# Kernel optimization log

Measured on AMD Instinct MI355X. Metric: run time of the kernel, lower is better.

## Reference

```python
import jax, jax.numpy as jnp
import numpy as np

N, C, B = 800000, 64, 8
BN_EPS = 1e-5


def setup_inputs() -> dict:
    key = jax.random.key(0)
    ks = jax.random.split(key, 8)
    x = jax.random.normal(ks[0], (N, C), dtype=jnp.float32)
    # cumulative end-offsets of B equal segments: [100000, 200000, ..., 800000]
    o = (jnp.arange(1, B + 1, dtype=jnp.int64) * (N // B))
    s2 = 1.0 / np.sqrt(C)
    s1 = 1.0 / np.sqrt(2 * C)
    w2 = jax.random.uniform(ks[1], (C, C), jnp.float32, -s2, s2)      # linear2 Linear(C,C)
    b2 = jax.random.uniform(ks[2], (C,), jnp.float32, -s2, s2)
    w1 = jax.random.uniform(ks[3], (C, 2 * C), jnp.float32, -s1, s1)  # linear1 Linear(2C,C)
    b1 = jax.random.uniform(ks[4], (C,), jnp.float32, -s1, s1)
    gamma = jnp.ones((C,), jnp.float32)   # BatchNorm1d weight
    beta = jnp.zeros((C,), jnp.float32)   # BatchNorm1d bias
    return {"x": x, "o": o, "w2": w2, "b2": b2, "w1": w1, "b1": b1,
            "gamma": gamma, "beta": beta}


def reference(x, o, w2, b2, w1, b1, gamma, beta):
    n = x.shape[0]
    nb = o.shape[0]
    # segment id of each point: point i belongs to segment j iff o[j-1] <= i < o[j]
    seg = jnp.searchsorted(o, jnp.arange(n), side="right")          # [N]
    counts = jnp.diff(o, prepend=0).astype(x.dtype)                  # [B]
    # per-segment mean pool
    means = jax.ops.segment_sum(x, seg, num_segments=nb) / counts[:, None]  # [B, C]
    # linear2: Linear + ReLU on pooled vectors
    h = jax.nn.relu(means @ w2.T + b2)                               # [B, C]
    # broadcast pooled features back to points and concat
    cat = jnp.concatenate([x, h[seg]], axis=1)                       # [N, 2C]
    # linear1: Linear + BatchNorm1d (training-mode batch stats) + ReLU
    y = cat @ w1.T + b1                                              # [N, C]
    mu = y.mean(axis=0)
    var = y.var(axis=0)
    y = (y - mu) * jax.lax.rsqrt(var + BN_EPS) * gamma + beta
    return jax.nn.relu(y)
```

## Files before the change

### kernel.cpp

```cpp
#include <hip/hip_runtime.h>

#define NROWS 800000
#define SEGROWS 100000
#define K1_BLOCKS 800
#define K1_ROWS 1000

typedef __attribute__((ext_vector_type(8))) short bf16x8;
typedef __attribute__((ext_vector_type(4))) float f32x4;
typedef __attribute__((ext_vector_type(4))) short short4v;

__device__ inline unsigned short f2bf(float f) {
    unsigned u = __builtin_bit_cast(unsigned, f);
    return (unsigned short)((u + 0x7FFFu + ((u >> 16) & 1u)) >> 16);
}

__global__ void kzero(float* __restrict__ p) {
    int t = blockIdx.x * 256 + threadIdx.x;
    if (t < 33280) p[t] = 0.f;
}

__global__ __launch_bounds__(256, 2)
void k1_stats(const float* __restrict__ x, float* __restrict__ m2p, float* __restrict__ ssumg)
{
    __shared__ __align__(16) float smem[5120];
    short* xt = (short*)smem;
    const float4* X4 = (const float4*)x;
    int t = threadIdx.x, w = t >> 6, lane = t & 63;
    int c4 = t & 15, g = t >> 4;
    size_t r0 = (size_t)blockIdx.x * K1_ROWS;
    int seg = (int)(r0 / SEGROWS);

    f32x4 acc[4][4];
#pragma unroll
    for (int p = 0; p < 4; ++p)
#pragma unroll
        for (int q = 0; q < 4; ++q) acc[p][q] = (f32x4){0.f, 0.f, 0.f, 0.f};
    float s0 = 0, s1 = 0, s2 = 0, s3 = 0;

    for (int tile = 0; tile < K1_ROWS; tile += 128) {
        int nr = min(128, K1_ROWS - tile);
        __syncthreads();
        if (nr == 128) {
            float4 v[8];
#pragma unroll
            for (int i = 0; i < 8; ++i)
                v[i] = X4[(r0 + tile + 8 * g + i) * 16 + c4];
#pragma unroll
            for (int i = 0; i < 8; ++i) {
                s0 += v[i].x; s1 += v[i].y; s2 += v[i].z; s3 += v[i].w;
            }
#pragma unroll
            for (int j = 0; j < 4; ++j) {
                bf16x8 pk;
#pragma unroll
                for (int i = 0; i < 8; ++i)
                    pk[i] = (short)f2bf(((const float*)&v[i])[j]);
                *(bf16x8*)&xt[(4 * c4 + j) * 136 + 8 * g] = pk;
            }
        } else {
#pragma unroll
            for (int h = 0; h < 2; ++h) {
                int rg = 8 * g + 4 * h;
                float4 v[4];
#pragma unroll
                for (int i = 0; i < 4; ++i) {
                    int r = rg + i;
                    if (r < nr) {
                        v[i] = X4[(r0 + tile + r) * 16 + c4];
                        s0 += v[i].x; s1 += v[i].y; s2 += v[i].z; s3 += v[i].w;
                    } else v[i] = make_float4(0.f, 0.f, 0.f, 0.f);
                }
#pragma unroll
                for (int j = 0; j < 4; ++j) {
                    short4v pk;
                    pk[0] = (short)f2bf(((const float*)&v[0])[j]);
                    pk[1] = (short)f2bf(((const float*)&v[1])[j]);
                    pk[2] = (short)f2bf(((const float*)&v[2])[j]);
                    pk[3] = (short)f2bf(((const float*)&v[3])[j]);
                    *(short4v*)&xt[(4 * c4 + j) * 136 + rg] = pk;
                }
            }
        }
        __syncthreads();
        bf16x8 f[4];
#pragma unroll
        for (int c0 = 0; c0 < 4; ++c0)
            f[c0] = *(const bf16x8*)&xt[(16 * c0 + (lane & 15)) * 136 + 32 * w + 8 * (lane >> 4)];
#pragma unroll
        for (int p = 0; p < 4; ++p)
#pragma unroll
            for (int q = 0; q < 4; ++q)
                acc[p][q] = __builtin_amdgcn_mfma_f32_16x16x32_bf16(f[p], f[q], acc[p][q], 0, 0, 0);
    }

    __syncthreads();
    ((float4*)(smem + 4096))[t] = make_float4(s0, s1, s2, s3);
    int qd = lane >> 4, cl = lane & 15;
    if (w == 0) {
#pragma unroll
        for (int p = 0; p < 4; ++p)
#pragma unroll
            for (int q = 0; q < 4; ++q)
#pragma unroll
                for (int i = 0; i < 4; ++i)
                    smem[(16 * p + 4 * qd + i) * 64 + 16 * q + cl] = acc[p][q][i];
    }
    __syncthreads();
    if (t < 64) {
        int cc4 = t >> 2, ii = t & 3;
        float s = 0;
#pragma unroll
        for (int u = 0; u < 16; ++u) s += smem[4096 + 4 * (cc4 + 16 * u) + ii];
        atomicAdd(&ssumg[seg * 64 + t], s);
    }
    for (int ww = 1; ww < 4; ++ww) {
        if (w == ww) {
#pragma unroll
            for (int p = 0; p < 4; ++p)
#pragma unroll
                for (int q = 0; q < 4; ++q)
#pragma unroll
                    for (int i = 0; i < 4; ++i)
                        smem[(16 * p + 4 * qd + i) * 64 + 16 * q + cl] += acc[p][q][i];
        }
        __syncthreads();
    }
    float* m2seg = m2p + seg * 4096;
#pragma unroll
    for (int ii = 0; ii < 16; ++ii) {
        int f2 = t + 256 * ((ii + blockIdx.x) & 15);
        atomicAdd(&m2seg[f2], smem[f2]);
    }
}

__global__ __launch_bounds__(256)
void k2b_solve(const int* __restrict__ o,
               const float* __restrict__ w2, const float* __restrict__ b2,
               const float* __restrict__ w1, const float* __restrict__ b1,
               const float* __restrict__ gamma, const float* __restrict__ beta,
               const float* __restrict__ m2p, const float* __restrict__ ssum,
               unsigned short* __restrict__ wpb, float* __restrict__ tbout)
{
    __shared__ __align__(16) float w1s[8192];
    __shared__ __align__(16) float w2s[4096];
    __shared__ __align__(16) float m2s[4096];
    __shared__ __align__(16) float ssums[512];
    __shared__ float means[512], hb[512], cv[512], q1p[256];
    __shared__ float Sx[64], muS[64], sS[64], cnts[8];

    int t = threadIdx.x;
    for (int i = t; i < 2048; i += 256) ((float4*)w1s)[i] = ((const float4*)w1)[i];
    for (int i = t; i < 1024; i += 256) ((float4*)w2s)[i] = ((const float4*)w2)[i];
    for (int i = t; i < 1024; i += 256) {
        float4 a = ((const float4*)m2p)[i];
#pragma unroll
        for (int s = 1; s < 8; ++s) {
            float4 b = ((const float4*)m2p)[s * 1024 + i];
            a.x += b.x; a.y += b.y; a.z += b.z; a.w += b.w;
        }
        ((float4*)m2s)[i] = a;
    }
    for (int i = t; i < 128;  i += 256) ((float4*)ssums)[i] = ((const float4*)ssum)[i];
    if (t < 8) cnts[t] = (float)(o[t] - (t ? o[t - 1] : 0));
    __syncthreads();

    for (int i = t; i < 512; i += 256) means[i] = ssums[i] / cnts[i >> 6];
    __syncthreads();
    int c = t & 63, g = t >> 6;
    for (int b = g; b < 8; b += 4) {
        float a = b2[c];
        for (int k = 0; k < 64; ++k) a = fmaf(means[b * 64 + k], w2s[c * 64 + k], a);
        hb[b * 64 + c] = fmaxf(a, 0.f);
    }
    __syncthreads();
    for (int b = g; b < 8; b += 4) {
        float a = b1[c];
        for (int k = 0; k < 64; ++k) a = fmaf(hb[b * 64 + k], w1s[c * 128 + 64 + k], a);
        cv[b * 64 + c] = a;
    }
    __syncthreads();
    if (t < 64) {
        float s = 0;
        for (int b = 0; b < 8; ++b) s += ssums[b * 64 + t];
        Sx[t] = s;
    }
    __syncthreads();
    {
        float p = 0;
        for (int j = g * 16; j < g * 16 + 16; ++j) {
            float vj = 0;
            for (int k = 0; k < 64; ++k) vj = fmaf(w1s[c * 128 + k], m2s[j * 64 + k], vj);
            p = fmaf(w1s[c * 128 + j], vj, p);
        }
        q1p[g * 64 + c] = p;
    }
    __syncthreads();
    if (t < 64) {
        const float Nf = (float)NROWS;
        float mu = 0;
        for (int k = 0; k < 64; ++k) mu = fmaf(w1s[t * 128 + k], Sx[k], mu);
        float q2 = 0, q3 = 0, msum = 0;
        for (int b = 0; b < 8; ++b) {
            float gv = cv[b * 64 + t];
            msum += cnts[b] * gv;
            q3 = fmaf(cnts[b] * gv, gv, q3);
            float dot = 0;
            for (int k = 0; k < 64; ++k) dot = fmaf(w1s[t * 128 + k], ssums[b * 64 + k], dot);
            q2 = fmaf(2.f * gv, dot, q2);
        }
        mu = (mu + msum) / Nf;
        float q1 = q1p[t] + q1p[64 + t] + q1p[128 + t] + q1p[192 + t];
        float var = (q1 + q2 + q3) / Nf - mu * mu;
        float s = gamma[t] * rsqrtf(var + 1e-5f);
        muS[t] = mu; sS[t] = s;
    }
    __syncthreads();
    for (int f = t; f < 4096; f += 256)
        wpb[f] = f2bf(w1s[(f >> 6) * 128 + (f & 63)] * sS[f >> 6]);
    for (int f = t; f < 512; f += 256)
        tbout[f] = (cv[f] - muS[f & 63]) * sS[f & 63] + beta[f & 63];
}

__global__ __launch_bounds__(256, 2)
void k3_gemm(const float* __restrict__ x, const unsigned short* __restrict__ wpb,
             const float* __restrict__ tb, float* __restrict__ out)
{
    __shared__ __align__(16) short bt[64 * 72];
    __shared__ float tbs[512];
    int t = threadIdx.x, lane = t & 63, w = t >> 6;
    size_t r0 = (size_t)blockIdx.x * 256;

    for (int f = t; f < 512; f += 256) {
        int c = f >> 3, kg = f & 7;
        uint4 vv = ((const uint4*)wpb)[f];
        *(uint4*)&bt[c * 72 + kg * 8] = vv;
    }
    for (int f = t; f < 512; f += 256) tbs[f] = tb[f];
    __syncthreads();

    int cl = lane & 15, qd = lane >> 4;
    int rbase = (int)r0 + 64 * w;

    float4 u[4][4];
#pragma unroll
    for (int m = 0; m < 4; ++m) {
        const float* rp = x + (size_t)(rbase + 16 * m + cl) * 64 + 8 * qd;
        u[m][0] = *(const float4*)(rp);
        u[m][1] = *(const float4*)(rp + 4);
        u[m][2] = *(const float4*)(rp + 32);
        u[m][3] = *(const float4*)(rp + 36);
    }

    bf16x8 B[4][2];
#pragma unroll
    for (int n = 0; n < 4; ++n)
#pragma unroll
        for (int k0 = 0; k0 < 2; ++k0)
            B[n][k0] = *(const bf16x8*)&bt[(16 * n + cl) * 72 + 32 * k0 + 8 * qd];

    f32x4 acc[4][4];
#pragma unroll
    for (int m = 0; m < 4; ++m)
#pragma unroll
        for (int n = 0; n < 4; ++n) acc[m][n] = (f32x4){0.f, 0.f, 0.f, 0.f};

#pragma unroll
    for (int m = 0; m < 4; ++m) {
        bf16x8 A0, A1;
        A0[0] = (short)f2bf(u[m][0].x); A0[1] = (short)f2bf(u[m][0].y);
        A0[2] = (short)f2bf(u[m][0].z); A0[3] = (short)f2bf(u[m][0].w);
        A0[4] = (short)f2bf(u[m][1].x); A0[5] = (short)f2bf(u[m][1].y);
        A0[6] = (short)f2bf(u[m][1].z); A0[7] = (short)f2bf(u[m][1].w);
        A1[0] = (short)f2bf(u[m][2].x); A1[1] = (short)f2bf(u[m][2].y);
        A1[2] = (short)f2bf(u[m][2].z); A1[3] = (short)f2bf(u[m][2].w);
        A1[4] = (short)f2bf(u[m][3].x); A1[5] = (short)f2bf(u[m][3].y);
        A1[6] = (short)f2bf(u[m][3].z); A1[7] = (short)f2bf(u[m][3].w);
#pragma unroll
        for (int n = 0; n < 4; ++n) {
            acc[m][n] = __builtin_amdgcn_mfma_f32_16x16x32_bf16(A0, B[n][0], acc[m][n], 0, 0, 0);
            acc[m][n] = __builtin_amdgcn_mfma_f32_16x16x32_bf16(A1, B[n][1], acc[m][n], 0, 0, 0);
        }
    }

    int seg0 = rbase / SEGROWS;
    int bnd = (seg0 + 1) * SEGROWS;
    int seg1 = min(seg0 + 1, 7);
    float tA[4], tB[4];
#pragma unroll
    for (int n = 0; n < 4; ++n) {
        tA[n] = tbs[seg0 * 64 + 16 * n + cl];
        tB[n] = tbs[seg1 * 64 + 16 * n + cl];
    }
#pragma unroll
    for (int m = 0; m < 4; ++m)
#pragma unroll
        for (int i = 0; i < 4; ++i) {
            int grow = rbase + 16 * m + 4 * qd + i;
            bool hi = grow >= bnd;
#pragma unroll
            for (int n = 0; n < 4; ++n) {
                float tv = hi ? tB[n] : tA[n];
                float vv = fmaxf(acc[m][n][i] + tv, 0.f);
                out[(size_t)grow * 64 + 16 * n + cl] = vv;
            }
        }
}

extern "C" void kernel_launch(void* const* d_in, const int* in_sizes, int n_in,
                              void* d_out, int out_size, void* d_ws, size_t ws_size,
                              hipStream_t stream)
{
    const float* x  = (const float*)d_in[0];
    const int*   o  = (const int*)d_in[1];
    const float* w2 = (const float*)d_in[2];
    const float* b2 = (const float*)d_in[3];
    const float* w1 = (const float*)d_in[4];
    const float* b1 = (const float*)d_in[5];
    const float* gm = (const float*)d_in[6];
    const float* bt = (const float*)d_in[7];
    float* out = (float*)d_out;
    float* ws  = (float*)d_ws;

    float*          m2p  = ws;
    float*          ssum = ws + 32768;
    float*          tbv  = ws + 33280;
    unsigned short* wpb  = (unsigned short*)(ws + 33792);

    kzero<<<130, 256, 0, stream>>>(ws);
    k1_stats<<<K1_BLOCKS, 256, 0, stream>>>(x, m2p, ssum);
    k2b_solve<<<1, 256, 0, stream>>>(o, w2, b2, w1, b1, gm, bt, m2p, ssum, wpb, tbv);
    k3_gemm<<<3125, 256, 0, stream>>>(x, wpb, tbv, out);
}
```

Before: 434.1 us.

## Load x directly into MFMA fragments, dropping LDS transpose staging in stats kernel

Measured after the change: 432.9 us. No clear change (-0.3%).

```diff
diff --git a/kernel.cpp b/kernel.cpp
--- a/kernel.cpp
+++ b/kernel.cpp
@@ -7,7 +7,6 @@
 
 typedef __attribute__((ext_vector_type(8))) short bf16x8;
 typedef __attribute__((ext_vector_type(4))) float f32x4;
-typedef __attribute__((ext_vector_type(4))) short short4v;
 
 __device__ inline unsigned short f2bf(float f) {
     unsigned u = __builtin_bit_cast(unsigned, f);
@@ -19,14 +18,13 @@
     if (t < 33280) p[t] = 0.f;
 }
 
-__global__ __launch_bounds__(256, 2)
+__global__ __launch_bounds__(256, 3)
 void k1_stats(const float* __restrict__ x, float* __restrict__ m2p, float* __restrict__ ssumg)
 {
-    __shared__ __align__(16) float smem[5120];
-    short* xt = (short*)smem;
-    const float4* X4 = (const float4*)x;
+    __shared__ __align__(16) float smem[4096];
+    __shared__ float red[4][256];
     int t = threadIdx.x, w = t >> 6, lane = t & 63;
-    int c4 = t & 15, g = t >> 4;
+    const int lg = lane >> 4, li = lane & 15;
     size_t r0 = (size_t)blockIdx.x * K1_ROWS;
     int seg = (int)(r0 / SEGROWS);
 
@@ -35,57 +33,33 @@
     for (int p = 0; p < 4; ++p)
 #pragma unroll
         for (int q = 0; q < 4; ++q) acc[p][q] = (f32x4){0.f, 0.f, 0.f, 0.f};
-    float s0 = 0, s1 = 0, s2 = 0, s3 = 0;
-
-    for (int tile = 0; tile < K1_ROWS; tile += 128) {
-        int nr = min(128, K1_ROWS - tile);
-        __syncthreads();
-        if (nr == 128) {
-            float4 v[8];
-#pragma unroll
-            for (int i = 0; i < 8; ++i)
-                v[i] = X4[(r0 + tile + 8 * g + i) * 16 + c4];
-#pragma unroll
-            for (int i = 0; i < 8; ++i) {
-                s0 += v[i].x; s1 += v[i].y; s2 += v[i].z; s3 += v[i].w;
+    float s[4] = {0.f, 0.f, 0.f, 0.f};
+
+    for (int ch = w; ch < 32; ch += 4) {
+        const int rb = 32 * ch + 8 * lg;
+        const float* xp = x + (r0 + rb) * 64 + li;
+        float xv[4][8];
+        if (ch < 31) {
+#pragma unroll
+            for (int c0 = 0; c0 < 4; ++c0)
+#pragma unroll
+                for (int j = 0; j < 8; ++j)
+                    xv[c0][j] = xp[(size_t)j * 64 + 16 * c0];
+        } else {
+#pragma unroll
+            for (int c0 = 0; c0 < 4; ++c0)
+#pragma unroll
+                for (int j = 0; j < 8; ++j)
+                    xv[c0][j] = (rb + j < K1_ROWS) ? xp[(size_t)j * 64 + 16 * c0] : 0.f;
+        }
+        bf16x8 f[4];
+#pragma unroll
+        for (int c0 = 0; c0 < 4; ++c0)
+#pragma unroll
+            for (int j = 0; j < 8; ++j) {
+                s[c0] += xv[c0][j];
+                f[c0][j] = (short)f2bf(xv[c0][j]);
             }
-#pragma unroll
-            for (int j = 0; j < 4; ++j) {
-                bf16x8 pk;
-#pragma unroll
-                for (int i = 0; i < 8; ++i)
-                    pk[i] = (short)f2bf(((const float*)&v[i])[j]);
-                *(bf16x8*)&xt[(4 * c4 + j) * 136 + 8 * g] = pk;
-            }
-        } else {
-#pragma unroll
-            for (int h = 0; h < 2; ++h) {
-                int rg = 8 * g + 4 * h;
-                float4 v[4];
-#pragma unroll
-                for (int i = 0; i < 4; ++i) {
-                    int r = rg + i;
-                    if (r < nr) {
-                        v[i] = X4[(r0 + tile + r) * 16 + c4];
-                        s0 += v[i].x; s1 += v[i].y; s2 += v[i].z; s3 += v[i].w;
-                    } else v[i] = make_float4(0.f, 0.f, 0.f, 0.f);
-                }
-#pragma unroll
-                for (int j = 0; j < 4; ++j) {
-                    short4v pk;
-                    pk[0] = (short)f2bf(((const float*)&v[0])[j]);
-                    pk[1] = (short)f2bf(((const float*)&v[1])[j]);
-                    pk[2] = (short)f2bf(((const float*)&v[2])[j]);
-                    pk[3] = (short)f2bf(((const float*)&v[3])[j]);
-                    *(short4v*)&xt[(4 * c4 + j) * 136 + rg] = pk;
-                }
-            }
-        }
-        __syncthreads();
-        bf16x8 f[4];
-#pragma unroll
-        for (int c0 = 0; c0 < 4; ++c0)
-            f[c0] = *(const bf16x8*)&xt[(16 * c0 + (lane & 15)) * 136 + 32 * w + 8 * (lane >> 4)];
 #pragma unroll
         for (int p = 0; p < 4; ++p)
 #pragma unroll
@@ -93,8 +67,8 @@
                 acc[p][q] = __builtin_amdgcn_mfma_f32_16x16x32_bf16(f[p], f[q], acc[p][q], 0, 0, 0);
     }
 
-    __syncthreads();
-    ((float4*)(smem + 4096))[t] = make_float4(s0, s1, s2, s3);
+#pragma unroll
+    for (int c0 = 0; c0 < 4; ++c0) red[c0][t] = s[c0];
     int qd = lane >> 4, cl = lane & 15;
     if (w == 0) {
 #pragma unroll
@@ -107,11 +81,12 @@
     }
     __syncthreads();
     if (t < 64) {
-        int cc4 = t >> 2, ii = t & 3;
-        float s = 0;
-#pragma unroll
-        for (int u = 0; u < 16; ++u) s += smem[4096 + 4 * (cc4 + 16 * u) + ii];
-        atomicAdd(&ssumg[seg * 64 + t], s);
+        int c0 = t >> 4, cc = t & 15;
+        float tot = 0;
+#pragma unroll
+        for (int u = 0; u < 16; ++u)
+            tot += red[c0][(u >> 2) * 64 + (u & 3) * 16 + cc];
+        atomicAdd(&ssumg[seg * 64 + t], tot);
     }
     for (int ww = 1; ww < 4; ++ww) {
         if (w == ww) {
```
